# Kernel optimization log

Hardware: AMD Instinct MI355X
Metric: run time of the kernel (lower is better)

The kernel has to match this reference:

```python
import jax, jax.numpy as jnp
import numpy as np

H, HKV, D, BS, NSEL, WIN = 32, 8, 64, 64, 16, 512
N_REP = H // HKV


def precompute_freqs(dim, max_seq_len, theta=10000.0):
    inv = 1.0 / theta ** (np.arange(0, dim, 2, dtype=np.float32) / dim)
    t = np.arange(max_seq_len, dtype=np.float32)
    return jnp.asarray(np.outer(t, inv))  # (S, dim//2)


def apply_rope(x, freqs):
    # x: (B, T, H, D)
    T = x.shape[1]
    xr = x.reshape(x.shape[:-1] + (-1, 2))
    cos = jnp.cos(freqs[:T])[None, :, None, :]
    sin = jnp.sin(freqs[:T])[None, :, None, :]
    x0, x1 = xr[..., 0], xr[..., 1]
    out = jnp.stack([x0 * cos - x1 * sin, x0 * sin + x1 * cos], axis=-1)
    return out.reshape(x.shape)


def setup_inputs() -> dict:
    key = jax.random.key(0)
    ks = jax.random.split(key, 9)
    d_model = 2048
    s = lambda fan_in: 1.0 / np.sqrt(fan_in)
    return {
        "x": jax.random.normal(ks[0], (1, 2048, d_model), jnp.float32),
        "W_q": jax.random.normal(ks[1], (d_model, H * D), jnp.float32) * s(d_model),
        "W_k": jax.random.normal(ks[2], (d_model, HKV * D), jnp.float32) * s(d_model),
        "W_v": jax.random.normal(ks[3], (d_model, HKV * D), jnp.float32) * s(d_model),
        "W_o": jax.random.normal(ks[4], (H * D, d_model), jnp.float32) * s(H * D),
        "W_ck": jax.random.normal(ks[5], (BS * D, D), jnp.float32) * s(BS * D),
        "W_cv": jax.random.normal(ks[6], (BS * D, D), jnp.float32) * s(BS * D),
        "W_imp": jax.random.normal(ks[7], (D, 1), jnp.float32) * s(D),
        "W_gate": jax.random.normal(ks[8], (d_model, 3), jnp.float32) * s(d_model),
    }


def reference(x, W_q, W_k, W_v, W_o, W_ck, W_cv, W_imp, W_gate):
    B, T, _ = x.shape
    S = T  # no kv_cache
    scale = 1.0 / np.sqrt(D)
    freqs = precompute_freqs(D, T)

    q = apply_rope((x @ W_q).reshape(B, T, H, D), freqs)
    k = apply_rope((x @ W_k).reshape(B, T, HKV, D), freqs)
    v = (x @ W_v).reshape(B, T, HKV, D)
    q = q.transpose(0, 2, 1, 3)  # (B,H,T,D)
    k = k.transpose(0, 2, 1, 3)  # (B,HKV,S,D)
    v = v.transpose(0, 2, 1, 3)

    # --- compressed-block branch ---
    nb = S // BS
    kb = k[:, :, : nb * BS].reshape(B, HKV, nb, BS * D)
    vb = v[:, :, : nb * BS].reshape(B, HKV, nb, BS * D)
    kc = jnp.repeat(kb @ W_ck, N_REP, axis=1)  # (B,H,nb,D)
    vc = jnp.repeat(vb @ W_cv, N_REP, axis=1)
    a_c = jax.nn.softmax(jnp.einsum('bhtd,bhnd->bhtn', q, kc) * scale, axis=-1)
    out_c = jnp.einsum('bhtn,bhnd->bhtd', a_c, vc)

    # GQA expansion shared by select / sliding branches
    kx = jnp.repeat(k, N_REP, axis=1)
    vx = jnp.repeat(v, N_REP, axis=1)

    # --- 'selected' branch (reference computes top-k indices but discards them;
    # attention is full dense unmasked softmax, faithfully reproduced) ---
    k_mean = k[:, :, : nb * BS].reshape(B, HKV, nb, BS, D).mean(axis=3)
    scores = (k_mean @ W_imp)[..., 0]
    _top = jax.lax.top_k(scores, NSEL)  # dead code in original; kept for faithfulness
    a_s = jax.nn.softmax(jnp.einsum('bhtd,bhsd->bhts', q, kx) * scale, axis=-1)
    out_s = jnp.einsum('bhts,bhsd->bhtd', a_s, vx)

    # --- sliding-window branch (dense scores + mask, as in original) ---
    logits = jnp.einsum('bhtd,bhsd->bhts', q, kx) * scale
    i = jnp.arange(T)[:, None]
    j = jnp.arange(S)[None, :]
    allowed = (j <= S - T + i) & (j >= S - T + i - WIN + 1)
    logits = jnp.where(allowed[None, None], logits, -jnp.inf)
    a_w = jnp.nan_to_num(jax.nn.softmax(logits, axis=-1))
    out_w = jnp.einsum('bhts,bhsd->bhtd', a_w, vx)

    # --- gated combine ---
    gates = jax.nn.softmax(x @ W_gate, axis=-1)  # (B,T,3)
    stacked = jnp.stack(
        [out_c.transpose(0, 2, 1, 3), out_s.transpose(0, 2, 1, 3), out_w.transpose(0, 2, 1, 3)],
        axis=3,
    )  # (B,T,H,3,D)
    out = (stacked * gates[:, :, None, :, None]).sum(axis=3).reshape(B, T, H * D)
    return out @ W_o
```

## Files before the change

### kernel.cpp

```cpp
#include <hip/hip_runtime.h>
#include <cmath>

typedef unsigned short u16;
typedef unsigned int u32;
typedef __attribute__((ext_vector_type(8))) __bf16 bf16x8;
typedef __attribute__((ext_vector_type(8))) u16 u16x8;
typedef __attribute__((ext_vector_type(4))) float f32x4;
typedef __attribute__((ext_vector_type(4))) u16 u16x4;

#define MFMA16(acc, a, b) (acc) = __builtin_amdgcn_mfma_f32_16x16x32_bf16((a), (b), (acc), 0, 0, 0)

__device__ __forceinline__ u16 f2bf(float x) {
  union { float f; u32 u; } c; c.f = x;
  u32 r = (c.u + 0x7FFFu + ((c.u >> 16) & 1u)) >> 16;
  return (u16)r;
}
__device__ __forceinline__ float bf2f(u16 b) {
  union { u32 u; float f; } c; c.u = ((u32)b) << 16;
  return c.f;
}
__device__ __forceinline__ float rowmax16(float v) {
#pragma unroll
  for (int m = 1; m < 16; m <<= 1) v = fmaxf(v, __shfl_xor(v, m));
  return v;
}
__device__ __forceinline__ float rowsum16(float v) {
#pragma unroll
  for (int m = 1; m < 16; m <<= 1) v += __shfl_xor(v, m);
  return v;
}
__device__ __forceinline__ void gload16(const u16* g, u16* l) {
  __builtin_amdgcn_global_load_lds(
      (const __attribute__((address_space(1))) void*)(g),
      (__attribute__((address_space(3))) void*)(l), 16, 0, 0);
}
__device__ __forceinline__ float exp2_asm(float x) {
  float r;
  asm("v_exp_f32 %0, %1\n\ts_nop 0" : "=v"(r) : "v"(x));
  return r;
}
__device__ __forceinline__ u32 cvtpk(float a, float b) {
  u32 r;
  asm("v_cvt_pk_bf16_f32 %0, %1, %2" : "=v"(r) : "v"(a), "v"(b));
  return r;
}
__device__ __forceinline__ u16x8 bc_u(bf16x8 v) { union { bf16x8 b; u16x8 u; } c; c.b = v; return c.u; }
__device__ __forceinline__ bf16x8 bc_b(u16x8 v) { union { u16x8 u; bf16x8 b; } c; c.u = v; return c.b; }
__device__ __forceinline__ bf16x8 pack8(f32x4 a, f32x4 b) {
  union { u32 w[4]; bf16x8 v; } c;
  c.w[0] = cvtpk(a[0], a[1]);
  c.w[1] = cvtpk(a[2], a[3]);
  c.w[2] = cvtpk(b[0], b[1]);
  c.w[3] = cvtpk(b[2], b[3]);
  return c.v;
}

__global__ void freqs_kernel(float* __restrict__ ct, float* __restrict__ st) {
  int idx = blockIdx.x * 256 + threadIdx.x;
  int t = idx >> 5, i = idx & 31;
  float inv = 1.0f / powf(10000.0f, (float)i / 32.0f);
  float a = (float)t * inv;
  float sv, cv;
  sincosf(a, &sv, &cv);
  ct[idx] = cv;
  st[idx] = sv;
}

__global__ void cvt_x_kernel(const float* __restrict__ in, u16* __restrict__ out) {
  int idx = (blockIdx.x * 256 + threadIdx.x) * 4;
  f32x4 v = *(const f32x4*)(in + idx);
  u16x4 o;
  o[0] = f2bf(v[0]); o[1] = f2bf(v[1]); o[2] = f2bf(v[2]); o[3] = f2bf(v[3]);
  *(u16x4*)(out + idx) = o;
}

__global__ __launch_bounds__(256) void trcvt_kernel(const float* __restrict__ W,
                                                    u16* __restrict__ Wt, int K, int N) {
  __shared__ u16 t_lds[64][65];
  int ntx = N >> 6;
  int kt = (blockIdx.x / ntx) * 64, nt = (blockIdx.x % ntx) * 64;
  int tx = threadIdx.x & 63, ty4 = threadIdx.x >> 6;
#pragma unroll 4
  for (int yy = 0; yy < 16; ++yy) {
    int k = kt + ty4 * 16 + yy;
    t_lds[ty4 * 16 + yy][tx] = f2bf(W[(size_t)k * N + nt + tx]);
  }
  __syncthreads();
#pragma unroll 4
  for (int yy = 0; yy < 16; ++yy) {
    int n = nt + ty4 * 16 + yy;
    Wt[(size_t)n * K + kt + tx] = t_lds[tx][ty4 * 16 + yy];
  }
}

__global__ __launch_bounds__(256) void gemm_bt_kernel(const u16* __restrict__ A,
                                                      const u16* __restrict__ Bt,
                                                      float* __restrict__ C,
                                                      int M, int N, int K) {
  __shared__ __align__(16) u16 As[128 * 64];
  __shared__ __align__(16) u16 Bs[128 * 64];
  const int tid = threadIdx.x;
  const int lane = tid & 63;
  const int w = tid >> 6;
  const int lr = lane & 15;
  const int lg = lane >> 4;
  const int lk8 = lg * 8;
  const int gx = gridDim.x;
  const int nwg = gx * gridDim.y;
  const int flat = blockIdx.y * gx + blockIdx.x;
  const int qq = nwg >> 3;
  const int swz = (flat & 7) * qq + (flat >> 3);
  const int brow = (swz % gx) * 128;
  const int bcol = (swz / gx) * 128;
  const int wr = (w >> 1) * 64;
  const int wc = (w & 1) * 64;

  const f32x4 zero4 = {0.f, 0.f, 0.f, 0.f};
  f32x4 acc[4][4];
#pragma unroll
  for (int m = 0; m < 4; ++m)
#pragma unroll
    for (int n = 0; n < 4; ++n) acc[m][n] = zero4;

  const int srow = tid >> 3;
  const int scol = (tid & 7) * 8;
  const u16* Ab = A + (size_t)(brow + srow) * K + scol;
  const u16* Bb = Bt + (size_t)(bcol + srow) * K + scol;

  for (int k0 = 0; k0 < K; k0 += 64) {
    __syncthreads();
#pragma unroll
    for (int it = 0; it < 4; ++it) {
      gload16(Ab + (size_t)it * 32 * K + k0, &As[tid * 8 + it * 2048]);
      gload16(Bb + (size_t)it * 32 * K + k0, &Bs[tid * 8 + it * 2048]);
    }
    __syncthreads();
#pragma unroll
    for (int kk = 0; kk < 2; ++kk) {
      bf16x8 af[4], bv[4];
#pragma unroll
      for (int m = 0; m < 4; ++m)
        af[m] = *(const bf16x8*)&As[(wr + m * 16 + lr) * 64 + kk * 32 + lk8];
#pragma unroll
      for (int n = 0; n < 4; ++n)
        bv[n] = *(const bf16x8*)&Bs[(wc + n * 16 + lr) * 64 + kk * 32 + lk8];
#pragma unroll
      for (int m = 0; m < 4; ++m)
#pragma unroll
        for (int n = 0; n < 4; ++n) MFMA16(acc[m][n], af[m], bv[n]);
    }
  }
#pragma unroll
  for (int m = 0; m < 4; ++m) {
#pragma unroll
    for (int rr = 0; rr < 4; ++rr) {
      int row = brow + wr + m * 16 + lg * 4 + rr;
#pragma unroll
      for (int n = 0; n < 4; ++n)
        C[(size_t)row * N + bcol + wc + n * 16 + lr] = acc[m][n][rr];
    }
  }
}

__global__ void rope_q_kernel(const float* __restrict__ qkv, const float* __restrict__ ct,
                              const float* __restrict__ st, u16* __restrict__ qb) {
  int idx = blockIdx.x * 256 + threadIdx.x;
  int i = idx & 31, hh = (idx >> 5) & 31, t = idx >> 10;
  float x0 = qkv[(size_t)t * 3072 + hh * 64 + 2 * i];
  float x1 = qkv[(size_t)t * 3072 + hh * 64 + 2 * i + 1];
  float c = ct[t * 32 + i], s = st[t * 32 + i];
  size_t o = ((size_t)hh * 2048 + t) * 64 + 2 * i;
  qb[o] = f2bf((x0 * c - x1 * s) * 0.125f);
  qb[o + 1] = f2bf((x0 * s + x1 * c) * 0.125f);
}
__global__ void rope_k_kernel(const float* __restrict__ qkv, const float* __restrict__ ct,
                              const float* __restrict__ st, u16* __restrict__ kb) {
  int idx = blockIdx.x * 256 + threadIdx.x;
  int i = idx & 31, hh = (idx >> 5) & 7, t = idx >> 8;
  float x0 = qkv[(size_t)t * 3072 + 2048 + hh * 64 + 2 * i];
  float x1 = qkv[(size_t)t * 3072 + 2048 + hh * 64 + 2 * i + 1];
  float c = ct[t * 32 + i], s = st[t * 32 + i];
  size_t o = ((size_t)hh * 2048 + t) * 64 + 2 * i;
  kb[o] = f2bf(x0 * c - x1 * s);
  kb[o + 1] = f2bf(x0 * s + x1 * c);
}
__global__ __launch_bounds__(256) void vtrans_kernel(const float* __restrict__ qkv,
                                                     u16* __restrict__ vbr,
                                                     u16* __restrict__ vb2) {
  __shared__ u16 tl[64][72];
  int hk = blockIdx.y, t0 = blockIdx.x * 64;
  int tx = threadIdx.x & 63, ty = threadIdx.x >> 6;
#pragma unroll 4
  for (int yy = 0; yy < 16; ++yy) {
    int row = ty * 16 + yy;
    u16 b = f2bf(qkv[(size_t)(t0 + row) * 3072 + 2560 + hk * 64 + tx]);
    tl[row][tx] = b;
    vbr[((size_t)hk * 2048 + t0 + row) * 64 + tx] = b;
  }
  __syncthreads();
  u16* dst = vb2 + (size_t)hk * 64 * 2048 + t0;
#pragma unroll 4
  for (int yy = 0; yy < 16; ++yy)
    dst[(size_t)(ty * 16 + yy) * 2048 + tx] = tl[tx][ty * 16 + yy];
}

__global__ __launch_bounds__(256) void gates_kernel(const float* __restrict__ x,
                                                    const float* __restrict__ Wg,
                                                    float* __restrict__ g) {
  int t = blockIdx.x * 4 + (threadIdx.x >> 6);
  int lane = threadIdx.x & 63;
  const float* xr = x + (size_t)t * 2048;
  float a0 = 0, a1 = 0, a2 = 0;
  for (int d = lane; d < 2048; d += 64) {
    float xv = xr[d];
    a0 = fmaf(xv, Wg[d * 3 + 0], a0);
    a1 = fmaf(xv, Wg[d * 3 + 1], a1);
    a2 = fmaf(xv, Wg[d * 3 + 2], a2);
  }
#pragma unroll
  for (int msk = 1; msk < 64; msk <<= 1) {
    a0 += __shfl_xor(a0, msk);
    a1 += __shfl_xor(a1, msk);
    a2 += __shfl_xor(a2, msk);
  }
  if (lane == 0) {
    float m = fmaxf(a0, fmaxf(a1, a2));
    float e0 = __expf(a0 - m), e1 = __expf(a1 - m), e2 = __expf(a2 - m);
    float inv = 1.f / (e0 + e1 + e2);
    g[t * 3 + 0] = e0 * inv; g[t * 3 + 1] = e1 * inv; g[t * 3 + 2] = e2 * inv;
  }
}

__global__ __launch_bounds__(256) void cgemm_kernel(const u16* __restrict__ kB,
                                                    const u16* __restrict__ vbr,
                                                    const float* __restrict__ Wck,
                                                    const float* __restrict__ Wcv,
                                                    float* __restrict__ kc,
                                                    float* __restrict__ vc) {
  __shared__ float red[4][64];
  int b = blockIdx.x;
  bool isv = b >= 256;
  int blk = b & 255;
  const u16* src = (isv ? vbr : kB) + (size_t)blk * 4096;
  const float* W = isv ? Wcv : Wck;
  float* out = (isv ? vc : kc) + (size_t)blk * 64;
  int lane = threadIdx.x & 63, w = threadIdx.x >> 6;
  int base = w * 1024;
  float acc0 = 0.f, acc1 = 0.f;
  for (int i = 0; i < 1024; i += 8) {
    u16x8 s8 = *(const u16x8*)(src + base + i);
#pragma unroll
    for (int j = 0; j < 8; j += 2) {
      acc0 = fmaf(bf2f(s8[j]), W[(size_t)(base + i + j) * 64 + lane], acc0);
      acc1 = fmaf(bf2f(s8[j + 1]), W[(size_t)(base + i + j + 1) * 64 + lane], acc1);
    }
  }
  red[w][lane] = acc0 + acc1;
  __syncthreads();
  if (w == 0)
    out[lane] = red[0][lane] + red[1][lane] + red[2][lane] + red[3][lane];
}

__global__ __launch_bounds__(256) void attn_kernel(
    const u16* __restrict__ qb, const u16* __restrict__ kb, const u16* __restrict__ vb2,
    const float* __restrict__ kcf, const float* __restrict__ vcf,
    const float* __restrict__ gf, u16* __restrict__ comb) {
  __shared__ __align__(16) u16 k_lds[2][64 * 64];
  __shared__ __align__(16) u16 vt_lds[2][64 * 64];
  __shared__ __align__(16) u16 p_lds[4][16 * 64];

  const int tid = threadIdx.x;
  const int lane = tid & 63;
  const int w = tid >> 6;
  const int lr = lane & 15;
  const int lg = lane >> 4;
  const int lk8 = lg * 8;
  const int h = blockIdx.y;
  const int hk = h >> 2;
  const int t0 = blockIdx.x * 64;
  const int tw = t0 + w * 16;
  const f32x4 zero4 = {0.f, 0.f, 0.f, 0.f};
  const float LOG2E = 1.44269504f;
  const float THR = 11.5416f;

  bf16x8 qf0, qf1;
  {
    const u16* qrow = qb + ((size_t)h * 2048 + (tw + lr)) * 64;
    qf0 = *(const bf16x8*)(qrow + lk8);
    qf1 = *(const bf16x8*)(qrow + 32 + lk8);
  }

  const int lin1 = 256 + tid;
  const int row0 = tid >> 3, sl0 = (tid & 7) ^ (row0 & 7);
  const int row1 = lin1 >> 3, sl1 = (lin1 & 7) ^ (row1 & 7);
  const u16* kS0 = kb + ((size_t)hk * 2048 + row0) * 64 + sl0 * 8;
  const u16* kS1 = kb + ((size_t)hk * 2048 + row1) * 64 + sl1 * 8;
  const u16* vS0 = vb2 + ((size_t)hk * 64 + row0) * 2048 + sl0 * 8;
  const u16* vS1 = vb2 + ((size_t)hk * 64 + row1) * 2048 + sl1 * 8;

  const int sA = ((0 + lg) ^ (lr & 7)) * 8;
  const int sB = ((4 + lg) ^ (lr & 7)) * 8;

  f32x4 acc_s[4], acc_w[4];
#pragma unroll
  for (int n = 0; n < 4; ++n) { acc_s[n] = zero4; acc_w[n] = zero4; }
  float m2[4], lsr[4], lwr[4];
#pragma unroll
  for (int r = 0; r < 4; ++r) { m2[r] = -1e30f; lsr[r] = 0.f; lwr[r] = 0.f; }

#define STAGE(cc)                                                      \
  {                                                                    \
    const int b_ = (cc) & 1;                                           \
    gload16(kS0 + (size_t)(cc) * 4096, &k_lds[b_][tid * 8]);           \
    gload16(kS1 + (size_t)(cc) * 4096, &k_lds[b_][2048 + tid * 8]);    \
    gload16(vS0 + (cc) * 64, &vt_lds[b_][tid * 8]);                    \
    gload16(vS1 + (cc) * 64, &vt_lds[b_][2048 + tid * 8]);             \
  }

  STAGE(0);
  __syncthreads();

#pragma unroll 1
  for (int c = 0; c < 32; ++c) {
    const int s0 = c * 64;
    const u16* kbuf = k_lds[c & 1];
    const u16* vbuf = vt_lds[c & 1];
    if (c < 31) STAGE(c + 1);

    f32x4 sc[4];
    __builtin_amdgcn_s_setprio(1);
#pragma unroll
    for (int cb = 0; cb < 4; ++cb) {
      f32x4 z = zero4;
      const int rb = (cb * 16 + lr) * 64;
      bf16x8 b0 = *(const bf16x8*)&kbuf[rb + sA];
      bf16x8 b1 = *(const bf16x8*)&kbuf[rb + sB];
      MFMA16(z, qf0, b0);
      MFMA16(z, qf1, b1);
      sc[cb] = z;
    }
    __builtin_amdgcn_s_setprio(0);

    const bool winAct = (s0 <= tw + 15) && (s0 + 63 >= tw - 511);
    const int dbase = tw + lg * 4 - s0 - lr;

    float mxl[4];
#pragma unroll
    for (int r = 0; r < 4; ++r)
      mxl[r] = fmaxf(fmaxf(sc[0][r], sc[1][r]), fmaxf(sc[2][r], sc[3][r]));
    float dmax = fmaxf(fmaxf(fmaf(mxl[0], LOG2E, -m2[0]), fmaf(mxl[1], LOG2E, -m2[1])),
                       fmaxf(fmaf(mxl[2], LOG2E, -m2[2]), fmaf(mxl[3], LOG2E, -m2[3])));
    if (__any(dmax > THR)) {
#pragma unroll
      for (int r = 0; r < 4; ++r) {
        float mnew = fmaxf(m2[r], rowmax16(mxl[r]) * LOG2E);
        float corr = exp2_asm(m2[r] - mnew);
        m2[r] = mnew;
        lsr[r] *= corr;
        lwr[r] *= corr;
#pragma unroll
        for (int n = 0; n < 4; ++n) { acc_s[n][r] *= corr; acc_w[n][r] *= corr; }
      }
    }

#pragma unroll
    for (int r = 0; r < 4; ++r) {
      float pv0 = exp2_asm(fmaf(sc[0][r], LOG2E, -m2[r]));
      float pv1 = exp2_asm(fmaf(sc[1][r], LOG2E, -m2[r]));
      float pv2 = exp2_asm(fmaf(sc[2][r], LOG2E, -m2[r]));
      float pv3 = exp2_asm(fmaf(sc[3][r], LOG2E, -m2[r]));
      lsr[r] += (pv0 + pv1) + (pv2 + pv3);
      if (winAct) {
        int d0 = dbase + r;
        float s = 0.f;
        s += ((u32)d0 < 512u) ? pv0 : 0.f;
        s += ((u32)(d0 - 16) < 512u) ? pv1 : 0.f;
        s += ((u32)(d0 - 32) < 512u) ? pv2 : 0.f;
        s += ((u32)(d0 - 48) < 512u) ? pv3 : 0.f;
        lwr[r] += s;
      }
      u32 pk01 = cvtpk(pv0, pv1), pk23 = cvtpk(pv2, pv3);
      const int prow = lg * 4 + r;
      const int pb = prow * 64 + (lr & 7);
      const int rh = prow & 7;
      const int shi = lr >> 3;
      u16* pl = p_lds[w];
      pl[pb + ((0 + shi) ^ rh) * 8] = (u16)pk01;
      pl[pb + ((2 + shi) ^ rh) * 8] = (u16)(pk01 >> 16);
      pl[pb + ((4 + shi) ^ rh) * 8] = (u16)pk23;
      pl[pb + ((6 + shi) ^ rh) * 8] = (u16)(pk23 >> 16);
    }
    asm volatile("s_waitcnt lgkmcnt(0)" ::: "memory");
    bf16x8 ap0 = *(const bf16x8*)&p_lds[w][lr * 64 + sA];
    bf16x8 ap1 = *(const bf16x8*)&p_lds[w][lr * 64 + sB];

    bf16x8 aw0 = ap0, aw1 = ap1;
    if (winAct) {
      const int base0 = (tw + lr) - (s0 + lk8);
      u16x8 a0 = bc_u(ap0), a1 = bc_u(ap1);
      u16x8 z0, z1;
#pragma unroll
      for (int j = 0; j < 8; ++j) {
        z0[j] = ((u32)(base0 - j) < 512u) ? a0[j] : (u16)0;
        z1[j] = ((u32)(base0 - 32 - j) < 512u) ? a1[j] : (u16)0;
      }
      aw0 = bc_b(z0);
      aw1 = bc_b(z1);
    }

    __builtin_amdgcn_s_setprio(1);
#pragma unroll
    for (int n = 0; n < 4; ++n) {
      const int rb = (n * 16 + lr) * 64;
      bf16x8 bv0 = *(const bf16x8*)&vbuf[rb + sA];
      bf16x8 bv1 = *(const bf16x8*)&vbuf[rb + sB];
      MFMA16(acc_s[n], ap0, bv0);
      MFMA16(acc_s[n], ap1, bv1);
      if (winAct) {
        MFMA16(acc_w[n], aw0, bv0);
        MFMA16(acc_w[n], aw1, bv1);
      }
    }
    __builtin_amdgcn_s_setprio(0);

    __syncthreads();
  }
#undef STAGE

  f32x4 accc[4];
  float lcv[4];
  {
    f32x4 sc0 = zero4, sc1 = zero4;
#pragma unroll
    for (int kk = 0; kk < 2; ++kk) {
      const float* kr0 = kcf + ((size_t)hk * 32 + 0 * 16 + lr) * 64 + kk * 32 + lk8;
      const float* kr1 = kcf + ((size_t)hk * 32 + 1 * 16 + lr) * 64 + kk * 32 + lk8;
      bf16x8 b0 = pack8(*(const f32x4*)kr0, *(const f32x4*)(kr0 + 4));
      bf16x8 b1 = pack8(*(const f32x4*)kr1, *(const f32x4*)(kr1 + 4));
      bf16x8 qk = kk ? qf1 : qf0;
      MFMA16(sc0, qk, b0);
      MFMA16(sc1, qk, b1);
    }
#pragma unroll
    for (int r = 0; r < 4; ++r) {
      float a = sc0[r], b = sc1[r];
      float m = rowmax16(fmaxf(a, b));
      float p0 = __expf(a - m), p1 = __expf(b - m);
      lcv[r] = rowsum16(p0 + p1);
      u32 pk = cvtpk(p0, p1);
      const int prow = lg * 4 + r;
      const int pb = prow * 64 + (lr & 7);
      const int rh = prow & 7;
      const int shi = lr >> 3;
      u16* pl = p_lds[w];
      pl[pb + ((0 + shi) ^ rh) * 8] = (u16)pk;
      pl[pb + ((2 + shi) ^ rh) * 8] = (u16)(pk >> 16);
    }
    asm volatile("s_waitcnt lgkmcnt(0)" ::: "memory");
    bf16x8 ap = *(const bf16x8*)&p_lds[w][lr * 64 + sA];
#pragma unroll
    for (int nb = 0; nb < 4; ++nb) {
      u16x8 bb;
#pragma unroll
      for (int j = 0; j < 8; ++j)
        bb[j] = f2bf(vcf[((size_t)hk * 32 + lk8 + j) * 64 + nb * 16 + lr]);
      f32x4 z = zero4;
      MFMA16(z, ap, bc_b(bb));
      accc[nb] = z;
    }
  }

#pragma unroll
  for (int r = 0; r < 4; ++r) {
    float ls = rowsum16(lsr[r]);
    float lw = rowsum16(lwr[r]);
    int t = tw + lg * 4 + r;
    float g0 = gf[t * 3 + 0], g1 = gf[t * 3 + 1], g2 = gf[t * 3 + 2];
    float wc_ = g0 / lcv[r];
    float ws_ = g1 / ls;
    float ww_ = g2 / lw;
#pragma unroll
    for (int n = 0; n < 4; ++n) {
      float val = accc[n][r] * wc_ + acc_s[n][r] * ws_ + acc_w[n][r] * ww_;
      comb[(size_t)t * 2048 + h * 64 + n * 16 + lr] = f2bf(val);
    }
  }
}

extern "C" void kernel_launch(void* const* d_in, const int* in_sizes, int n_in,
                              void* d_out, int out_size, void* d_ws, size_t ws_size,
                              hipStream_t stream) {
  (void)in_sizes; (void)n_in; (void)out_size;
  const float* x   = (const float*)d_in[0];
  const float* Wq  = (const float*)d_in[1];
  const float* Wk  = (const float*)d_in[2];
  const float* Wv  = (const float*)d_in[3];
  const float* Wo  = (const float*)d_in[4];
  const float* Wck = (const float*)d_in[5];
  const float* Wcv = (const float*)d_in[6];
  const float* Wg  = (const float*)d_in[8];
  float* out = (float*)d_out;
  char* ws = (char*)d_ws;

  constexpr size_t OXB   = 0;
  constexpr size_t OWT   = OXB  + 8388608;
  constexpr size_t OWOT  = OWT  + 12582912;
  constexpr size_t OQKV  = OWOT + 8388608;
  constexpr size_t OQB   = OQKV + 25165824;
  constexpr size_t OKB   = OQB  + 8388608;
  constexpr size_t OVB   = OKB  + 2097152;
  constexpr size_t OCT   = OVB  + 2097152;
  constexpr size_t OST   = OCT  + 262144;
  constexpr size_t OKC   = OST  + 262144;
  constexpr size_t OVC   = OKC  + 65536;
  constexpr size_t OG    = OVC  + 65536;
  constexpr size_t OCOMB = OG   + 24576;
  constexpr size_t TOTAL = OCOMB + 8388608;
  if (ws_size < TOTAL) return;

  u16* xb    = (u16*)(ws + OXB);
  u16* WT    = (u16*)(ws + OWT);
  u16* WoT   = (u16*)(ws + OWOT);
  float* qkv = (float*)(ws + OQKV);
  u16* qB    = (u16*)(ws + OQB);
  u16* kB    = (u16*)(ws + OKB);
  u16* vB2   = (u16*)(ws + OVB);
  float* ct  = (float*)(ws + OCT);
  float* st  = (float*)(ws + OST);
  float* kc  = (float*)(ws + OKC);
  float* vc  = (float*)(ws + OVC);
  float* gg  = (float*)(ws + OG);
  u16* comb  = (u16*)(ws + OCOMB);
  u16* vbr   = comb;

  freqs_kernel<<<dim3(256), dim3(256), 0, stream>>>(ct, st);
  cvt_x_kernel<<<dim3(4096), dim3(256), 0, stream>>>(x, xb);
  trcvt_kernel<<<dim3(1024), dim3(256), 0, stream>>>(Wq, WT, 2048, 2048);
  trcvt_kernel<<<dim3(256),  dim3(256), 0, stream>>>(Wk, WT + (size_t)2048 * 2048, 2048, 512);
  trcvt_kernel<<<dim3(256),  dim3(256), 0, stream>>>(Wv, WT + (size_t)2560 * 2048, 2048, 512);
  trcvt_kernel<<<dim3(1024), dim3(256), 0, stream>>>(Wo, WoT, 2048, 2048);

  gemm_bt_kernel<<<dim3(16, 24), dim3(256), 0, stream>>>(xb, WT, qkv, 2048, 3072, 2048);

  rope_q_kernel<<<dim3(8192), dim3(256), 0, stream>>>(qkv, ct, st, qB);
  rope_k_kernel<<<dim3(2048), dim3(256), 0, stream>>>(qkv, ct, st, kB);
  vtrans_kernel<<<dim3(32, 8), dim3(256), 0, stream>>>(qkv, vbr, vB2);
  gates_kernel<<<dim3(512), dim3(256), 0, stream>>>(x, Wg, gg);

  cgemm_kernel<<<dim3(512), dim3(256), 0, stream>>>(kB, vbr, Wck, Wcv, kc, vc);

  attn_kernel<<<dim3(32, 32), dim3(256), 0, stream>>>(qB, kB, vB2, kc, vc, gg, comb);

  gemm_bt_kernel<<<dim3(16, 16), dim3(256), 0, stream>>>(comb, WoT, out, 2048, 2048, 2048);
}
```

Measured before the change: 282.2 us.

## Load K/V fragments directly from global memory and swizzle block-to-head mapping

```diff
diff --git a/kernel.cpp b/kernel.cpp
--- a/kernel.cpp
+++ b/kernel.cpp
@@ -265,8 +265,6 @@
     const u16* __restrict__ qb, const u16* __restrict__ kb, const u16* __restrict__ vb2,
     const float* __restrict__ kcf, const float* __restrict__ vcf,
     const float* __restrict__ gf, u16* __restrict__ comb) {
-  __shared__ __align__(16) u16 k_lds[2][64 * 64];
-  __shared__ __align__(16) u16 vt_lds[2][64 * 64];
   __shared__ __align__(16) u16 p_lds[4][16 * 64];
 
   const int tid = threadIdx.x;
@@ -275,9 +273,11 @@
   const int lr = lane & 15;
   const int lg = lane >> 4;
   const int lk8 = lg * 8;
-  const int h = blockIdx.y;
+  const int flat = blockIdx.y * gridDim.x + blockIdx.x;
+  const int swz = (flat & 7) * 128 + (flat >> 3);
+  const int h = swz >> 5;
+  const int t0 = (swz & 31) * 64;
   const int hk = h >> 2;
-  const int t0 = blockIdx.x * 64;
   const int tw = t0 + w * 16;
   const f32x4 zero4 = {0.f, 0.f, 0.f, 0.f};
   const float LOG2E = 1.44269504f;
@@ -290,13 +290,8 @@
     qf1 = *(const bf16x8*)(qrow + 32 + lk8);
   }
 
-  const int lin1 = 256 + tid;
-  const int row0 = tid >> 3, sl0 = (tid & 7) ^ (row0 & 7);
-  const int row1 = lin1 >> 3, sl1 = (lin1 & 7) ^ (row1 & 7);
-  const u16* kS0 = kb + ((size_t)hk * 2048 + row0) * 64 + sl0 * 8;
-  const u16* kS1 = kb + ((size_t)hk * 2048 + row1) * 64 + sl1 * 8;
-  const u16* vS0 = vb2 + ((size_t)hk * 64 + row0) * 2048 + sl0 * 8;
-  const u16* vS1 = vb2 + ((size_t)hk * 64 + row1) * 2048 + sl1 * 8;
+  const u16* kbase = kb + (size_t)hk * 2048 * 64;
+  const u16* vbase = vb2 + (size_t)hk * 64 * 2048;
 
   const int sA = ((0 + lg) ^ (lr & 7)) * 8;
   const int sB = ((4 + lg) ^ (lr & 7)) * 8;
@@ -307,34 +302,19 @@
   float m2[4], lsr[4], lwr[4];
 #pragma unroll
   for (int r = 0; r < 4; ++r) { m2[r] = -1e30f; lsr[r] = 0.f; lwr[r] = 0.f; }
-
-#define STAGE(cc)                                                      \
-  {                                                                    \
-    const int b_ = (cc) & 1;                                           \
-    gload16(kS0 + (size_t)(cc) * 4096, &k_lds[b_][tid * 8]);           \
-    gload16(kS1 + (size_t)(cc) * 4096, &k_lds[b_][2048 + tid * 8]);    \
-    gload16(vS0 + (cc) * 64, &vt_lds[b_][tid * 8]);                    \
-    gload16(vS1 + (cc) * 64, &vt_lds[b_][2048 + tid * 8]);             \
-  }
-
-  STAGE(0);
-  __syncthreads();
 
 #pragma unroll 1
   for (int c = 0; c < 32; ++c) {
     const int s0 = c * 64;
-    const u16* kbuf = k_lds[c & 1];
-    const u16* vbuf = vt_lds[c & 1];
-    if (c < 31) STAGE(c + 1);
 
     f32x4 sc[4];
     __builtin_amdgcn_s_setprio(1);
 #pragma unroll
     for (int cb = 0; cb < 4; ++cb) {
+      const u16* krow = kbase + (size_t)(s0 + cb * 16 + lr) * 64;
+      bf16x8 b0 = *(const bf16x8*)(krow + lk8);
+      bf16x8 b1 = *(const bf16x8*)(krow + 32 + lk8);
       f32x4 z = zero4;
-      const int rb = (cb * 16 + lr) * 64;
-      bf16x8 b0 = *(const bf16x8*)&kbuf[rb + sA];
-      bf16x8 b1 = *(const bf16x8*)&kbuf[rb + sB];
       MFMA16(z, qf0, b0);
       MFMA16(z, qf1, b1);
       sc[cb] = z;
@@ -411,9 +391,9 @@
     __builtin_amdgcn_s_setprio(1);
 #pragma unroll
     for (int n = 0; n < 4; ++n) {
-      const int rb = (n * 16 + lr) * 64;
-      bf16x8 bv0 = *(const bf16x8*)&vbuf[rb + sA];
-      bf16x8 bv1 = *(const bf16x8*)&vbuf[rb + sB];
+      const u16* vrow = vbase + (size_t)(n * 16 + lr) * 2048 + s0;
+      bf16x8 bv0 = *(const bf16x8*)(vrow + lk8);
+      bf16x8 bv1 = *(const bf16x8*)(vrow + 32 + lk8);
       MFMA16(acc_s[n], ap0, bv0);
       MFMA16(acc_s[n], ap1, bv1);
       if (winAct) {
@@ -422,10 +402,7 @@
       }
     }
     __builtin_amdgcn_s_setprio(0);
-
-    __syncthreads();
-  }
-#undef STAGE
+  }
 
   f32x4 accc[4];
   float lcv[4];
```

Result: slower. 408.5 us (+44.7%).
